# Performance work log

Hardware: AMD Instinct MI355X
Metric: run time of the kernel (lower is better)

## Reference

```python
import jax, jax.numpy as jnp
import numpy as np

N, E, D, H = 50000, 800000, 128, 4
DH = D // H  # head dim = 32


def setup_inputs() -> dict:
    key = jax.random.key(0)
    ks = jax.random.split(key, 16)
    inp = {
        "node_feats": jax.random.normal(ks[0], (N, D), jnp.float32),
        "edge_feats": jax.random.normal(ks[1], (E, D), jnp.float32),
        "src": jax.random.randint(ks[2], (E,), 0, N, jnp.int32),
        "dst": jax.random.randint(ks[3], (E,), 0, N, jnp.int32),
        # MHA projections (no bias since num_input == num_output feats)
        "Wq": jax.random.normal(ks[4], (D, D), jnp.float32) / np.sqrt(D),
        "Wk": jax.random.normal(ks[5], (D, D), jnp.float32) / np.sqrt(D),
        "Wv": jax.random.normal(ks[6], (D, D), jnp.float32) / np.sqrt(D),
        "We": jax.random.normal(ks[7], (D, D), jnp.float32) / np.sqrt(D),
        # output projection (with bias)
        "O_w": jax.random.normal(ks[8], (D, D), jnp.float32) / np.sqrt(D),
        "O_b": jnp.zeros((D,), jnp.float32),
        # batch-norm affine params
        "g1n": jnp.ones((D,), jnp.float32), "b1n": jnp.zeros((D,), jnp.float32),
        "g1e": jnp.ones((D,), jnp.float32), "b1e": jnp.zeros((D,), jnp.float32),
        "g2": jnp.ones((D,), jnp.float32), "b2": jnp.zeros((D,), jnp.float32),
        # node-feats MLP (no bias)
        "W1": jax.random.normal(ks[9], (D, 2 * D), jnp.float32) / np.sqrt(D),
        "W2": jax.random.normal(ks[10], (2 * D, D), jnp.float32) / np.sqrt(2 * D),
    }
    return inp


def _batch_norm(x, gamma, beta, eps=1e-5):
    # training-style BatchNorm1d: biased variance over the batch (node/edge) dim
    mean = jnp.mean(x, axis=0)
    var = jnp.var(x, axis=0)
    return (x - mean) * jax.lax.rsqrt(var + eps) * gamma + beta


def reference(node_feats, edge_feats, src, dst, Wq, Wk, Wv, We, O_w, O_b,
              g1n, b1n, g1e, b1e, g2, b2, W1, W2):
    h_in1 = node_feats
    nf = _batch_norm(node_feats, g1n, b1n)
    ef = _batch_norm(edge_feats, g1e, b1e)

    Q = (nf @ Wq).reshape(N, H, DH)
    K = (nf @ Wk).reshape(N, H, DH)
    V = (nf @ Wv).reshape(N, H, DH)
    proj_e = (ef @ We).reshape(E, H, DH)

    # edge-wise multiplicative attention: [E, H, DH]
    score = jnp.clip(K[src] * Q[dst] / np.sqrt(DH).astype(np.float32), -5.0, 5.0) * proj_e
    s = jnp.exp(jnp.clip(jnp.sum(score, axis=-1, keepdims=True), -5.0, 5.0))  # [E, H, 1]

    # scatter-sum aggregation to destination nodes
    wV = jax.ops.segment_sum(s * V[src], dst, num_segments=N)  # [N, H, DH]
    z = jax.ops.segment_sum(s, dst, num_segments=N)            # [N, H, 1]
    h = (wV / (z + 1e-6)).reshape(N, D)

    # dropout is identity in eval mode
    h = h @ O_w + O_b
    h = h_in1 + h  # residual 1

    h_in2 = h
    h = _batch_norm(h, g2, b2)
    h = jax.nn.silu(h @ W1) @ W2  # node_feats_MLP (dropout = identity)
    h = h_in2 + h  # residual 2
    return h
```

## Files before the change

kernel.cpp:

```cpp
#include <hip/hip_runtime.h>
#include <hip/hip_bf16.h>
#include <math.h>

#define N_NODES 50000
#define N_EDGES 800000
#define DIM 128
#define NH 4

typedef __attribute__((ext_vector_type(8))) short bf16x8;
typedef __attribute__((ext_vector_type(4))) float f32x4;
typedef unsigned int uint;
typedef unsigned short ushort;

__device__ inline short f2bf(float f) {
  __hip_bfloat16 h = __float2bfloat16(f);
  return __builtin_bit_cast(short, h);
}
__device__ inline uint pack_bf2(float lo, float hi) {
  return (uint)(ushort)f2bf(lo) | ((uint)(ushort)f2bf(hi) << 16);
}
__device__ inline float bflo(uint u) { return __builtin_bit_cast(float, u << 16); }
__device__ inline float bfhi(uint u) { return __builtin_bit_cast(float, u & 0xffff0000u); }

__global__ __launch_bounds__(256) void bn_stats_kernel(
    const float* __restrict__ x, int M, float* __restrict__ out) {
  __shared__ float s_sum[DIM];
  __shared__ float s_sq[DIM];
  int t = threadIdx.x;
  if (t < DIM) { s_sum[t] = 0.f; s_sq[t] = 0.f; }
  __syncthreads();
  int c4 = (t & 31) * 4;
  int rg = t >> 5;
  float sum0=0,sum1=0,sum2=0,sum3=0, sq0=0,sq1=0,sq2=0,sq3=0;
  for (long row = (long)blockIdx.x * 8 + rg; row < M; row += (long)gridDim.x * 8) {
    float4 v = *reinterpret_cast<const float4*>(x + row * DIM + c4);
    sum0 += v.x; sq0 += v.x * v.x;
    sum1 += v.y; sq1 += v.y * v.y;
    sum2 += v.z; sq2 += v.z * v.z;
    sum3 += v.w; sq3 += v.w * v.w;
  }
  atomicAdd(&s_sum[c4 + 0], sum0); atomicAdd(&s_sq[c4 + 0], sq0);
  atomicAdd(&s_sum[c4 + 1], sum1); atomicAdd(&s_sq[c4 + 1], sq1);
  atomicAdd(&s_sum[c4 + 2], sum2); atomicAdd(&s_sq[c4 + 2], sq2);
  atomicAdd(&s_sum[c4 + 3], sum3); atomicAdd(&s_sq[c4 + 3], sq3);
  __syncthreads();
  if (t < DIM) {
    atomicAdd(&out[t], s_sum[t]);
    atomicAdd(&out[DIM + t], s_sq[t]);
  }
}

__global__ __launch_bounds__(256) void bn_stats_hist_kernel(
    const float* __restrict__ x, const int* __restrict__ dst,
    float* __restrict__ out, int* __restrict__ deg) {
  __shared__ float s_sum[DIM];
  __shared__ float s_sq[DIM];
  int t = threadIdx.x;
  if (t < DIM) { s_sum[t] = 0.f; s_sq[t] = 0.f; }
  __syncthreads();
  for (long i = (long)blockIdx.x * 256 + t; i < N_EDGES; i += (long)gridDim.x * 256) {
    atomicAdd(&deg[dst[i]], 1);
  }
  int c4 = (t & 31) * 4;
  int rg = t >> 5;
  float sum0=0,sum1=0,sum2=0,sum3=0, sq0=0,sq1=0,sq2=0,sq3=0;
  for (long row = (long)blockIdx.x * 8 + rg; row < N_EDGES; row += (long)gridDim.x * 8) {
    float4 v = *reinterpret_cast<const float4*>(x + row * DIM + c4);
    sum0 += v.x; sq0 += v.x * v.x;
    sum1 += v.y; sq1 += v.y * v.y;
    sum2 += v.z; sq2 += v.z * v.z;
    sum3 += v.w; sq3 += v.w * v.w;
  }
  atomicAdd(&s_sum[c4 + 0], sum0); atomicAdd(&s_sq[c4 + 0], sq0);
  atomicAdd(&s_sum[c4 + 1], sum1); atomicAdd(&s_sq[c4 + 1], sq1);
  atomicAdd(&s_sum[c4 + 2], sum2); atomicAdd(&s_sq[c4 + 2], sq2);
  atomicAdd(&s_sum[c4 + 3], sum3); atomicAdd(&s_sq[c4 + 3], sq3);
  __syncthreads();
  if (t < DIM) {
    atomicAdd(&out[t], s_sum[t]);
    atomicAdd(&out[DIM + t], s_sq[t]);
  }
}

__global__ __launch_bounds__(1024) void fold6_kernel(
    const float* __restrict__ Wq, const float* __restrict__ Wk,
    const float* __restrict__ Wv, const float* __restrict__ We,
    const float* __restrict__ Ow, const float* __restrict__ W2,
    const float* __restrict__ stats_n, const float* __restrict__ stats_e,
    const float* __restrict__ g1n, const float* __restrict__ b1n,
    const float* __restrict__ g1e, const float* __restrict__ b1e, float inv_s,
    short* __restrict__ WqT, short* __restrict__ WkT,
    short* __restrict__ WvT, short* __restrict__ WeT,
    short* __restrict__ OwT, short* __restrict__ W2T,
    float* __restrict__ bq, float* __restrict__ bk,
    float* __restrict__ bv, float* __restrict__ be) {
  int b = blockIdx.x;
  int t = threadIdx.x;
  if (b == 4) {
    int d = t & 127, kg = t >> 7;
#pragma unroll
    for (int j = 0; j < 16; ++j) {
      int k = kg * 16 + j;
      OwT[d * DIM + k] = f2bf(Ow[k * DIM + d]);
    }
    return;
  }
  if (b == 5) {
    int d = t & 127, kg = t >> 7;
#pragma unroll
    for (int j = 0; j < 32; ++j) {
      int k = kg * 32 + j;
      W2T[d * 256 + k] = f2bf(W2[k * DIM + d]);
    }
    return;
  }
  __shared__ float red[8][DIM];
  __shared__ float sab[DIM], sbb[DIM];
  const float* W = (b == 0) ? Wq : (b == 1) ? Wk : (b == 2) ? Wv : We;
  const float* stats = (b == 3) ? stats_e : stats_n;
  const float* gamma = (b == 3) ? g1e : g1n;
  const float* beta  = (b == 3) ? b1e : b1n;
  float M            = (b == 3) ? (float)N_EDGES : (float)N_NODES;
  float scale = (b == 1) ? inv_s : 1.f;
  short* WT = (b == 0) ? WqT : (b == 1) ? WkT : (b == 2) ? WvT : WeT;
  float* bias = (b == 0) ? bq : (b == 1) ? bk : (b == 2) ? bv : be;
  if (t < DIM) {
    float mean = stats[t] / M;
    float var = stats[DIM + t] / M - mean * mean;
    float a = gamma[t] * rsqrtf(var + 1e-5f);
    sab[t] = a;
    sbb[t] = beta[t] - mean * a;
  }
  __syncthreads();
  int d = t & 127, kg = t >> 7;
  int ct = d >> 4, lr = d & 15;
  int L = (ct >> 1) * 32 + lr * 2 + (ct & 1);
  float bacc = 0.f;
#pragma unroll
  for (int j = 0; j < 16; ++j) {
    int k = kg * 16 + j;
    float wv = W[k * DIM + L];
    WT[d * DIM + k] = f2bf(scale * sab[k] * wv);
    bacc += sbb[k] * wv;
  }
  red[kg][d] = bacc;
  __syncthreads();
  if (kg == 0) {
    float s = 0.f;
#pragma unroll
    for (int j = 0; j < 8; ++j) s += red[j][d];
    bias[d] = scale * s;
  }
}

__global__ __launch_bounds__(256) void fold_w1_kernel(
    const float* __restrict__ W1, const float* __restrict__ stats_h,
    const float* __restrict__ g2, const float* __restrict__ b2,
    short* __restrict__ W1F, float* __restrict__ bias1) {
  __shared__ float sab[DIM], sbb[DIM];
  int t = threadIdx.x;
  if (t < DIM) {
    float mean = stats_h[t] / (float)N_NODES;
    float var = stats_h[DIM + t] / (float)N_NODES - mean * mean;
    float a = g2[t] * rsqrtf(var + 1e-5f);
    sab[t] = a;
    sbb[t] = b2[t] - mean * a;
  }
  __syncthreads();
  float bacc = 0.f;
  for (int k = 0; k < DIM; ++k) {
    float wv = W1[k * 256 + t];
    W1F[t * DIM + k] = f2bf(sab[k] * wv);
    bacc += sbb[k] * wv;
  }
  bias1[t] = bacc;
}

__device__ inline void load_a_frags(const float* __restrict__ X, long m0,
                                    int lr, int lg, bf16x8 a[4]) {
#pragma unroll
  for (int ks = 0; ks < 4; ++ks) {
    const float* p = X + (m0 + lr) * DIM + ks * 32 + lg * 8;
    float4 v0 = *reinterpret_cast<const float4*>(p);
    float4 v1 = *reinterpret_cast<const float4*>(p + 4);
    bf16x8 af;
    af[0] = f2bf(v0.x); af[1] = f2bf(v0.y); af[2] = f2bf(v0.z); af[3] = f2bf(v0.w);
    af[4] = f2bf(v1.x); af[5] = f2bf(v1.y); af[6] = f2bf(v1.z); af[7] = f2bf(v1.w);
    a[ks] = af;
  }
}

__global__ __launch_bounds__(256) void qkv_mfma_kernel(
    const float* __restrict__ nf,
    const short* __restrict__ WqT, const short* __restrict__ WkT, const short* __restrict__ WvT,
    const float* __restrict__ bq, const float* __restrict__ bk, const float* __restrict__ bv,
    ushort* __restrict__ Qb, ushort* __restrict__ Kb, ushort* __restrict__ Vb) {
  int t = threadIdx.x;
  int w = t >> 6, l = t & 63;
  int lr = l & 15, lg = l >> 4;
  long m0 = (long)blockIdx.x * 64 + w * 16;
  if (m0 >= N_NODES) return;
  bf16x8 a[4];
  load_a_frags(nf, m0, lr, lg, a);
  const short* Ws[3] = {WqT, WkT, WvT};
  const float* bs[3] = {bq, bk, bv};
  ushort* Os[3] = {Qb, Kb, Vb};
#pragma unroll 1
  for (int m = 0; m < 3; ++m) {
    const short* WT = Ws[m];
    f32x4 acc[8];
#pragma unroll
    for (int ct = 0; ct < 8; ++ct) acc[ct] = (f32x4){0.f, 0.f, 0.f, 0.f};
#pragma unroll
    for (int ct = 0; ct < 8; ++ct) {
#pragma unroll
      for (int ks = 0; ks < 4; ++ks) {
        bf16x8 b = *reinterpret_cast<const bf16x8*>(WT + (ct * 16 + lr) * DIM + ks * 32 + lg * 8);
        acc[ct] = __builtin_amdgcn_mfma_f32_16x16x32_bf16(a[ks], b, acc[ct], 0, 0, 0);
      }
    }
    const float* bb = bs[m];
    ushort* O = Os[m];
#pragma unroll
    for (int h = 0; h < 4; ++h) {
      float b0 = bb[(2 * h) * 16 + lr];
      float b1 = bb[(2 * h + 1) * 16 + lr];
#pragma unroll
      for (int r = 0; r < 4; ++r) {
        uint u = pack_bf2(acc[2 * h][r] + b0, acc[2 * h + 1][r] + b1);
        *reinterpret_cast<uint*>(O + (m0 + lg * 4 + r) * DIM + h * 32 + lr * 2) = u;
      }
    }
  }
}

#define SCAN_T 1024
#define PER_T 49
__global__ __launch_bounds__(SCAN_T) void scan_kernel(
    const int* __restrict__ deg, int* __restrict__ row_start, int* __restrict__ cursor) {
  __shared__ int ps[SCAN_T];
  int t = threadIdx.x;
  int base = t * PER_T;
  int lsum = 0;
  int local[PER_T];
#pragma unroll
  for (int j = 0; j < PER_T; ++j) {
    int idx = base + j;
    int d = (idx < N_NODES) ? deg[idx] : 0;
    local[j] = lsum;
    lsum += d;
  }
  ps[t] = lsum;
  __syncthreads();
  for (int off = 1; off < SCAN_T; off <<= 1) {
    int v = (t >= off) ? ps[t - off] : 0;
    __syncthreads();
    ps[t] += v;
    __syncthreads();
  }
  int prefix = (t == 0) ? 0 : ps[t - 1];
#pragma unroll
  for (int j = 0; j < PER_T; ++j) {
    int idx = base + j;
    if (idx < N_NODES) {
      int v = prefix + local[j];
      row_start[idx] = v;
      cursor[idx] = v;
    }
  }
  if (t == SCAN_T - 1) row_start[N_NODES] = ps[SCAN_T - 1];
}

__global__ __launch_bounds__(256) void scatter_kernel(
    const int* __restrict__ src, const int* __restrict__ dst,
    int* __restrict__ cursor, int2* __restrict__ csr) {
  int i = blockIdx.x * 256 + threadIdx.x;
  int d = dst[i];
  int pos = atomicAdd(&cursor[d], 1);
  csr[pos] = make_int2(src[i], i);
}

#define ES_GRID 2048
__global__ __launch_bounds__(256) void edge_score_kernel(
    const float* __restrict__ ef,
    const int* __restrict__ src, const int* __restrict__ dst,
    const short* __restrict__ WeT, const float* __restrict__ be,
    const ushort* __restrict__ Qb, const ushort* __restrict__ Kb,
    float* __restrict__ s_out) {
  const int NT = N_EDGES / 64;
  int t = threadIdx.x;
  int w = t >> 6, l = t & 63;
  int lr = l & 15, lg = l >> 4;
  int stride = gridDim.x;
  float ber[8];
#pragma unroll
  for (int ct = 0; ct < 8; ++ct) ber[ct] = be[ct * 16 + lr];

  int tile = blockIdx.x;
  int4 s4, d4;
  f32x4 af[8];
  {
    long m0 = (long)tile * 64 + w * 16;
    long eb = m0 + lg * 4;
    s4 = *reinterpret_cast<const int4*>(src + eb);
    d4 = *reinterpret_cast<const int4*>(dst + eb);
#pragma unroll
    for (int ks = 0; ks < 4; ++ks) {
      const float* p = ef + (m0 + lr) * DIM + ks * 32 + lg * 8;
      af[2 * ks]     = __builtin_nontemporal_load(reinterpret_cast<const f32x4*>(p));
      af[2 * ks + 1] = __builtin_nontemporal_load(reinterpret_cast<const f32x4*>(p + 4));
    }
  }

#pragma unroll 2
  for (; tile < NT; tile += stride) {
    int pt = (tile + stride < NT) ? (tile + stride) : (NT - 1);
    int sn[4] = {s4.x, s4.y, s4.z, s4.w};
    int dn[4] = {d4.x, d4.y, d4.z, d4.w};
    uint Kg[4][4], Qg[4][4];
#pragma unroll
    for (int r = 0; r < 4; ++r) {
#pragma unroll
      for (int h = 0; h < 4; ++h) {
        Kg[r][h] = *reinterpret_cast<const uint*>(Kb + (long)sn[r] * DIM + h * 32 + lr * 2);
        Qg[r][h] = *reinterpret_cast<const uint*>(Qb + (long)dn[r] * DIM + h * 32 + lr * 2);
      }
    }
    long pm0 = (long)pt * 64 + w * 16;
    long peb = pm0 + lg * 4;
    int4 ns4 = *reinterpret_cast<const int4*>(src + peb);
    int4 nd4 = *reinterpret_cast<const int4*>(dst + peb);
    bf16x8 a[4];
#pragma unroll
    for (int ks = 0; ks < 4; ++ks) {
      f32x4 v0 = af[2 * ks], v1 = af[2 * ks + 1];
      bf16x8 t8;
      t8[0] = f2bf(v0.x); t8[1] = f2bf(v0.y); t8[2] = f2bf(v0.z); t8[3] = f2bf(v0.w);
      t8[4] = f2bf(v1.x); t8[5] = f2bf(v1.y); t8[6] = f2bf(v1.z); t8[7] = f2bf(v1.w);
      a[ks] = t8;
    }
    f32x4 naf[8];
#pragma unroll
    for (int ks = 0; ks < 4; ++ks) {
      const float* p = ef + (pm0 + lr) * DIM + ks * 32 + lg * 8;
      naf[2 * ks]     = __builtin_nontemporal_load(reinterpret_cast<const f32x4*>(p));
      naf[2 * ks + 1] = __builtin_nontemporal_load(reinterpret_cast<const f32x4*>(p + 4));
    }
    f32x4 acc[8];
#pragma unroll
    for (int ct = 0; ct < 8; ++ct) acc[ct] = (f32x4){0.f, 0.f, 0.f, 0.f};
#pragma unroll
    for (int ct = 0; ct < 8; ++ct) {
#pragma unroll
      for (int ks = 0; ks < 4; ++ks) {
        bf16x8 b = *reinterpret_cast<const bf16x8*>(WeT + (ct * 16 + lr) * DIM + ks * 32 + lg * 8);
        acc[ct] = __builtin_amdgcn_mfma_f32_16x16x32_bf16(a[ks], b, acc[ct], 0, 0, 0);
      }
    }
    long eb = (long)tile * 64 + w * 16 + lg * 4;
#pragma unroll
    for (int r = 0; r < 4; ++r) {
      float hs0, hs1, hs2, hs3;
      {
        float h0, h1, h2, h3;
#pragma unroll
        for (int h = 0; h < 4; ++h) {
          float k0 = bflo(Kg[r][h]), k1 = bfhi(Kg[r][h]);
          float q0 = bflo(Qg[r][h]), q1 = bfhi(Qg[r][h]);
          float pe0 = acc[2 * h][r] + ber[2 * h];
          float pe1 = acc[2 * h + 1][r] + ber[2 * h + 1];
          float v = fminf(fmaxf(k0 * q0, -5.f), 5.f) * pe0
                  + fminf(fmaxf(k1 * q1, -5.f), 5.f) * pe1;
          if (h == 0) h0 = v; else if (h == 1) h1 = v; else if (h == 2) h2 = v; else h3 = v;
        }
        hs0 = h0; hs1 = h1; hs2 = h2; hs3 = h3;
      }
#pragma unroll
      for (int m2 = 8; m2 >= 1; m2 >>= 1) {
        hs0 += __shfl_xor(hs0, m2);
        hs1 += __shfl_xor(hs1, m2);
        hs2 += __shfl_xor(hs2, m2);
        hs3 += __shfl_xor(hs3, m2);
      }
      if (lr < 4) {
        float myh = (lr == 0) ? hs0 : ((lr == 1) ? hs1 : ((lr == 2) ? hs2 : hs3));
        s_out[(eb + r) * 4 + lr] = __expf(fminf(fmaxf(myh, -5.f), 5.f));
      }
    }
    s4 = ns4; d4 = nd4;
#pragma unroll
    for (int i = 0; i < 8; ++i) af[i] = naf[i];
  }
}

__global__ __launch_bounds__(256) void aggregate_kernel(
    const int* __restrict__ row_start, const int2* __restrict__ csr,
    const float* __restrict__ s_arr, const ushort* __restrict__ Vb,
    ushort* __restrict__ haggb) {
  int t = threadIdx.x;
  int w = t >> 6, l = t & 63;
  int n = blockIdx.x * 4 + w;
  int r0 = row_start[n], r1 = row_start[n + 1];
  int h = l >> 4;
  float a0 = 0.f, a1 = 0.f, zacc = 0.f;
  int idx = r0;
  for (; idx + 4 <= r1; idx += 4) {
    int2 rec[4];
#pragma unroll
    for (int j = 0; j < 4; ++j) rec[j] = csr[idx + j];
    float sv[4]; uint uv[4];
#pragma unroll
    for (int j = 0; j < 4; ++j) {
      sv[j] = s_arr[(long)rec[j].y * 4 + h];
      uv[j] = *reinterpret_cast<const uint*>(Vb + (long)rec[j].x * DIM + l * 2);
    }
#pragma unroll
    for (int j = 0; j < 4; ++j) {
      a0 += sv[j] * bflo(uv[j]);
      a1 += sv[j] * bfhi(uv[j]);
      zacc += sv[j];
    }
  }
  for (; idx < r1; ++idx) {
    int2 ra = csr[idx];
    float sa = s_arr[(long)ra.y * 4 + h];
    uint ua = *reinterpret_cast<const uint*>(Vb + (long)ra.x * DIM + l * 2);
    a0 += sa * bflo(ua);
    a1 += sa * bfhi(ua);
    zacc += sa;
  }
  float inv = 1.f / (zacc + 1e-6f);
  *reinterpret_cast<uint*>(haggb + (long)n * DIM + l * 2) = pack_bf2(a0 * inv, a1 * inv);
}

__global__ __launch_bounds__(256) void attnout_mfma_kernel(
    const ushort* __restrict__ haggb, const short* __restrict__ OwT,
    const float* __restrict__ Ob, const float* __restrict__ h_in1,
    float* __restrict__ hres, float* __restrict__ stats2) {
  int t = threadIdx.x;
  int w = t >> 6, l = t & 63;
  int lr = l & 15, lg = l >> 4;
  long m0 = (long)blockIdx.x * 64 + w * 16;
  if (m0 >= N_NODES) return;
  bf16x8 a[4];
#pragma unroll
  for (int ks = 0; ks < 4; ++ks) {
    a[ks] = *reinterpret_cast<const bf16x8*>(haggb + (m0 + lr) * DIM + ks * 32 + lg * 8);
  }
  f32x4 acc[8];
#pragma unroll
  for (int ct = 0; ct < 8; ++ct) acc[ct] = (f32x4){0.f, 0.f, 0.f, 0.f};
#pragma unroll
  for (int ct = 0; ct < 8; ++ct) {
#pragma unroll
    for (int ks = 0; ks < 4; ++ks) {
      bf16x8 b = *reinterpret_cast<const bf16x8*>(OwT + (ct * 16 + lr) * DIM + ks * 32 + lg * 8);
      acc[ct] = __builtin_amdgcn_mfma_f32_16x16x32_bf16(a[ks], b, acc[ct], 0, 0, 0);
    }
  }
#pragma unroll
  for (int ct = 0; ct < 8; ++ct) {
    float ob = Ob[ct * 16 + lr];
    float ls = 0.f, lq = 0.f;
#pragma unroll
    for (int r = 0; r < 4; ++r) {
      long idx = (m0 + lg * 4 + r) * DIM + ct * 16 + lr;
      float hv = h_in1[idx] + acc[ct][r] + ob;
      hres[idx] = hv;
      ls += hv; lq += hv * hv;
    }
    ls += __shfl_xor(ls, 16); ls += __shfl_xor(ls, 32);
    lq += __shfl_xor(lq, 16); lq += __shfl_xor(lq, 32);
    if (lg == 0) {
      atomicAdd(&stats2[ct * 16 + lr], ls);
      atomicAdd(&stats2[DIM + ct * 16 + lr], lq);
    }
  }
}

__global__ __launch_bounds__(256) void mlp_mfma_kernel(
    const float* __restrict__ hres, const short* __restrict__ W1F,
    const float* __restrict__ bias1, const short* __restrict__ W2T,
    float* __restrict__ out) {
  __shared__ short mid[64][264];
  int t = threadIdx.x;
  int w = t >> 6, l = t & 63;
  int lr = l & 15, lg = l >> 4;
  long m0 = (long)blockIdx.x * 64 + w * 16;
  if (m0 >= N_NODES) return;
  bf16x8 a1[4];
  load_a_frags(hres, m0, lr, lg, a1);
#pragma unroll
  for (int ct = 0; ct < 16; ++ct) {
    f32x4 acc = (f32x4){0.f, 0.f, 0.f, 0.f};
#pragma unroll
    for (int ks = 0; ks < 4; ++ks) {
      bf16x8 b = *reinterpret_cast<const bf16x8*>(W1F + (ct * 16 + lr) * DIM + ks * 32 + lg * 8);
      acc = __builtin_amdgcn_mfma_f32_16x16x32_bf16(a1[ks], b, acc, 0, 0, 0);
    }
    float bb = bias1[ct * 16 + lr];
#pragma unroll
    for (int r = 0; r < 4; ++r) {
      float x = acc[r] + bb;
      float sl = x / (1.f + __expf(-x));
      mid[w * 16 + lg * 4 + r][ct * 16 + lr] = f2bf(sl);
    }
  }
  bf16x8 a2[8];
#pragma unroll
  for (int ks = 0; ks < 8; ++ks) {
    a2[ks] = *reinterpret_cast<const bf16x8*>(&mid[w * 16 + lr][ks * 32 + lg * 8]);
  }
#pragma unroll
  for (int ct = 0; ct < 8; ++ct) {
    f32x4 acc = (f32x4){0.f, 0.f, 0.f, 0.f};
#pragma unroll
    for (int ks = 0; ks < 8; ++ks) {
      bf16x8 b = *reinterpret_cast<const bf16x8*>(W2T + (ct * 16 + lr) * 256 + ks * 32 + lg * 8);
      acc = __builtin_amdgcn_mfma_f32_16x16x32_bf16(a2[ks], b, acc, 0, 0, 0);
    }
#pragma unroll
    for (int r = 0; r < 4; ++r) {
      long idx = (m0 + lg * 4 + r) * DIM + ct * 16 + lr;
      out[idx] = hres[idx] + acc[r];
    }
  }
}

extern "C" void kernel_launch(void* const* d_in, const int* in_sizes, int n_in,
                              void* d_out, int out_size, void* d_ws, size_t ws_size,
                              hipStream_t stream) {
  const float* node_feats = (const float*)d_in[0];
  const float* edge_feats = (const float*)d_in[1];
  const int* src = (const int*)d_in[2];
  const int* dst = (const int*)d_in[3];
  const float* Wq = (const float*)d_in[4];
  const float* Wk = (const float*)d_in[5];
  const float* Wv = (const float*)d_in[6];
  const float* We = (const float*)d_in[7];
  const float* Ow = (const float*)d_in[8];
  const float* Ob = (const float*)d_in[9];
  const float* g1n = (const float*)d_in[10];
  const float* b1n = (const float*)d_in[11];
  const float* g1e = (const float*)d_in[12];
  const float* b1e = (const float*)d_in[13];
  const float* g2 = (const float*)d_in[14];
  const float* b2 = (const float*)d_in[15];
  const float* W1 = (const float*)d_in[16];
  const float* W2 = (const float*)d_in[17];
  float* out = (float*)d_out;
  float* w = (float*)d_ws;

  float* stats_n = w + 0;
  float* stats_e = w + 256;
  float* stats_h = w + 512;
  float* bq = w + 1536;
  float* bk = w + 1664;
  float* bv = w + 1792;
  float* be = w + 1920;
  short* WqT = (short*)(w + 2048);
  short* WkT = (short*)(w + 10240);
  short* WvT = (short*)(w + 18432);
  short* WeT = (short*)(w + 26624);
  short* OwT = (short*)(w + 34816);
  short* W1F = (short*)(w + 43008);
  short* W2T = (short*)(w + 59392);
  float* bias1 = w + 75776;
  ushort* Qb = (ushort*)(w + 76032);
  ushort* Kb = (ushort*)(w + 3276032);
  ushort* Vb = (ushort*)(w + 6476032);
  float* s_arr = w + 9676032;
  int* deg = (int*)(w + 12876032);
  int* row_start = deg + 50048;
  int* cursor = row_start + 50064;
  int2* csr = (int2*)(cursor + 50048);
  ushort* haggb = (ushort*)(w + 76032);

  const float inv_s = 0.17677669529663687f;

  hipMemsetAsync(w, 0, 768 * sizeof(float), stream);
  hipMemsetAsync(deg, 0, 50000 * sizeof(int), stream);

  bn_stats_kernel<<<512, 256, 0, stream>>>(node_feats, N_NODES, stats_n);
  bn_stats_hist_kernel<<<2048, 256, 0, stream>>>(edge_feats, dst, stats_e, deg);
  fold6_kernel<<<6, 1024, 0, stream>>>(Wq, Wk, Wv, We, Ow, W2, stats_n, stats_e,
                                       g1n, b1n, g1e, b1e, inv_s,
                                       WqT, WkT, WvT, WeT, OwT, W2T, bq, bk, bv, be);
  scan_kernel<<<1, SCAN_T, 0, stream>>>(deg, row_start, cursor);
  scatter_kernel<<<N_EDGES / 256, 256, 0, stream>>>(src, dst, cursor, csr);

  qkv_mfma_kernel<<<(N_NODES + 63) / 64, 256, 0, stream>>>(
      node_feats, WqT, WkT, WvT, bq, bk, bv, Qb, Kb, Vb);
  edge_score_kernel<<<ES_GRID, 256, 0, stream>>>(
      edge_feats, src, dst, WeT, be, Qb, Kb, s_arr);
  aggregate_kernel<<<N_NODES / 4, 256, 0, stream>>>(row_start, csr, s_arr, Vb, haggb);
  attnout_mfma_kernel<<<(N_NODES + 63) / 64, 256, 0, stream>>>(
      haggb, OwT, Ob, node_feats, out, stats_h);
  fold_w1_kernel<<<1, 256, 0, stream>>>(W1, stats_h, g2, b2, W1F, bias1);
  mlp_mfma_kernel<<<(N_NODES + 63) / 64, 256, 0, stream>>>(out, W1F, bias1, W2T, out);
}
```

Measured before the change: 814.4 us.

## Deepen edge-score gather pipeline and parallelize W1 folding across blocks

The edge score loop now software-pipelines the Q/K gathers one tile ahead and the src/dst index loads two tiles ahead, so random gather latency overlaps the current tile's MFMA work. The edge-feature prefetch writes directly into the live register buffer instead of a temporary copy. The W1 fold kernel is spread from one block to 16 blocks, each reducing partial bias sums in shared memory, to shorten a serial single-block step. The deeper pipeline raises register pressure and may reduce occupancy.

```diff
diff --git a/kernel.cpp b/kernel.cpp
--- a/kernel.cpp
+++ b/kernel.cpp
@@ -158,6 +158,7 @@
     const float* __restrict__ g2, const float* __restrict__ b2,
     short* __restrict__ W1F, float* __restrict__ bias1) {
   __shared__ float sab[DIM], sbb[DIM];
+  __shared__ float red[16][17];
   int t = threadIdx.x;
   if (t < DIM) {
     float mean = stats_h[t] / (float)N_NODES;
@@ -167,13 +168,24 @@
     sbb[t] = b2[t] - mean * a;
   }
   __syncthreads();
+  int dl = t & 15, kg = t >> 4;
+  int d = blockIdx.x * 16 + dl;
   float bacc = 0.f;
-  for (int k = 0; k < DIM; ++k) {
-    float wv = W1[k * 256 + t];
-    W1F[t * DIM + k] = f2bf(sab[k] * wv);
+#pragma unroll
+  for (int j = 0; j < 8; ++j) {
+    int k = kg * 8 + j;
+    float wv = W1[k * 256 + d];
+    W1F[d * DIM + k] = f2bf(sab[k] * wv);
     bacc += sbb[k] * wv;
   }
-  bias1[t] = bacc;
+  red[dl][kg] = bacc;
+  __syncthreads();
+  if (kg == 0) {
+    float s = 0.f;
+#pragma unroll
+    for (int j = 0; j < 16; ++j) s += red[dl][j];
+    bias1[d] = s;
+  }
 }
 
 __device__ inline void load_a_frags(const float* __restrict__ X, long m0,
@@ -297,13 +309,12 @@
   for (int ct = 0; ct < 8; ++ct) ber[ct] = be[ct * 16 + lr];
 
   int tile = blockIdx.x;
-  int4 s4, d4;
+  long sb0 = (long)tile * 64 + w * 16 + lg * 4;
+  int4 s4 = *reinterpret_cast<const int4*>(src + sb0);
+  int4 d4 = *reinterpret_cast<const int4*>(dst + sb0);
   f32x4 af[8];
   {
     long m0 = (long)tile * 64 + w * 16;
-    long eb = m0 + lg * 4;
-    s4 = *reinterpret_cast<const int4*>(src + eb);
-    d4 = *reinterpret_cast<const int4*>(dst + eb);
 #pragma unroll
     for (int ks = 0; ks < 4; ++ks) {
       const float* p = ef + (m0 + lr) * DIM + ks * 32 + lg * 8;
@@ -311,25 +322,28 @@
       af[2 * ks + 1] = __builtin_nontemporal_load(reinterpret_cast<const f32x4*>(p + 4));
     }
   }
-
-#pragma unroll 2
-  for (; tile < NT; tile += stride) {
-    int pt = (tile + stride < NT) ? (tile + stride) : (NT - 1);
+  uint KgA[4][4], QgA[4][4];
+  {
     int sn[4] = {s4.x, s4.y, s4.z, s4.w};
     int dn[4] = {d4.x, d4.y, d4.z, d4.w};
-    uint Kg[4][4], Qg[4][4];
 #pragma unroll
     for (int r = 0; r < 4; ++r) {
 #pragma unroll
       for (int h = 0; h < 4; ++h) {
-        Kg[r][h] = *reinterpret_cast<const uint*>(Kb + (long)sn[r] * DIM + h * 32 + lr * 2);
-        Qg[r][h] = *reinterpret_cast<const uint*>(Qb + (long)dn[r] * DIM + h * 32 + lr * 2);
-      }
-    }
-    long pm0 = (long)pt * 64 + w * 16;
-    long peb = pm0 + lg * 4;
-    int4 ns4 = *reinterpret_cast<const int4*>(src + peb);
-    int4 nd4 = *reinterpret_cast<const int4*>(dst + peb);
+        KgA[r][h] = *reinterpret_cast<const uint*>(Kb + (long)sn[r] * DIM + h * 32 + lr * 2);
+        QgA[r][h] = *reinterpret_cast<const uint*>(Qb + (long)dn[r] * DIM + h * 32 + lr * 2);
+      }
+    }
+  }
+  int t1 = (tile + stride < NT) ? tile + stride : NT - 1;
+  long sb1 = (long)t1 * 64 + w * 16 + lg * 4;
+  int4 s4n = *reinterpret_cast<const int4*>(src + sb1);
+  int4 d4n = *reinterpret_cast<const int4*>(dst + sb1);
+
+  for (; tile < NT; tile += stride) {
+    int ptile = (tile + stride < NT) ? tile + stride : NT - 1;
+    int pptile = (tile + 2 * stride < NT) ? tile + 2 * stride : NT - 1;
+    long pm0 = (long)ptile * 64 + w * 16;
     bf16x8 a[4];
 #pragma unroll
     for (int ks = 0; ks < 4; ++ks) {
@@ -339,13 +353,28 @@
       t8[4] = f2bf(v1.x); t8[5] = f2bf(v1.y); t8[6] = f2bf(v1.z); t8[7] = f2bf(v1.w);
       a[ks] = t8;
     }
-    f32x4 naf[8];
 #pragma unroll
     for (int ks = 0; ks < 4; ++ks) {
       const float* p = ef + (pm0 + lr) * DIM + ks * 32 + lg * 8;
-      naf[2 * ks]     = __builtin_nontemporal_load(reinterpret_cast<const f32x4*>(p));
-      naf[2 * ks + 1] = __builtin_nontemporal_load(reinterpret_cast<const f32x4*>(p + 4));
-    }
+      af[2 * ks]     = __builtin_nontemporal_load(reinterpret_cast<const f32x4*>(p));
+      af[2 * ks + 1] = __builtin_nontemporal_load(reinterpret_cast<const f32x4*>(p + 4));
+    }
+    uint KgB[4][4], QgB[4][4];
+    {
+      int sn[4] = {s4n.x, s4n.y, s4n.z, s4n.w};
+      int dn[4] = {d4n.x, d4n.y, d4n.z, d4n.w};
+#pragma unroll
+      for (int r = 0; r < 4; ++r) {
+#pragma unroll
+        for (int h = 0; h < 4; ++h) {
+          KgB[r][h] = *reinterpret_cast<const uint*>(Kb + (long)sn[r] * DIM + h * 32 + lr * 2);
+          QgB[r][h] = *reinterpret_cast<const uint*>(Qb + (long)dn[r] * DIM + h * 32 + lr * 2);
+        }
+      }
+    }
+    long sb2 = (long)pptile * 64 + w * 16 + lg * 4;
+    int4 s4nn = *reinterpret_cast<const int4*>(src + sb2);
+    int4 d4nn = *reinterpret_cast<const int4*>(dst + sb2);
     f32x4 acc[8];
 #pragma unroll
     for (int ct = 0; ct < 8; ++ct) acc[ct] = (f32x4){0.f, 0.f, 0.f, 0.f};
@@ -365,8 +394,8 @@
         float h0, h1, h2, h3;
 #pragma unroll
         for (int h = 0; h < 4; ++h) {
-          float k0 = bflo(Kg[r][h]), k1 = bfhi(Kg[r][h]);
-          float q0 = bflo(Qg[r][h]), q1 = bfhi(Qg[r][h]);
+          float k0 = bflo(KgA[r][h]), k1 = bfhi(KgA[r][h]);
+          float q0 = bflo(QgA[r][h]), q1 = bfhi(QgA[r][h]);
           float pe0 = acc[2 * h][r] + ber[2 * h];
           float pe1 = acc[2 * h + 1][r] + ber[2 * h + 1];
           float v = fminf(fmaxf(k0 * q0, -5.f), 5.f) * pe0
@@ -387,9 +416,12 @@
         s_out[(eb + r) * 4 + lr] = __expf(fminf(fmaxf(myh, -5.f), 5.f));
       }
     }
-    s4 = ns4; d4 = nd4;
-#pragma unroll
-    for (int i = 0; i < 8; ++i) af[i] = naf[i];
+#pragma unroll
+    for (int r = 0; r < 4; ++r) {
+#pragma unroll
+      for (int h = 0; h < 4; ++h) { KgA[r][h] = KgB[r][h]; QgA[r][h] = QgB[r][h]; }
+    }
+    s4n = s4nn; d4n = d4nn;
   }
 }
 
@@ -596,6 +628,6 @@
   aggregate_kernel<<<N_NODES / 4, 256, 0, stream>>>(row_start, csr, s_arr, Vb, haggb);
   attnout_mfma_kernel<<<(N_NODES + 63) / 64, 256, 0, stream>>>(
       haggb, OwT, Ob, node_feats, out, stats_h);
-  fold_w1_kernel<<<1, 256, 0, stream>>>(W1, stats_h, g2, b2, W1F, bias1);
+  fold_w1_kernel<<<16, 256, 0, stream>>>(W1, stats_h, g2, b2, W1F, bias1);
   mlp_mfma_kernel<<<(N_NODES + 63) / 64, 256, 0, stream>>>(out, W1F, bias1, W2T, out);
 }
```

Result: no change. 815.1 us (+0.1%).

## Process edges in CSR order and parallelize W1 folding across blocks

Applied to the files above, without the earlier changes.

The scatter kernel now writes an int4 record (src, edge id, dst) per CSR slot. The edge-score kernel walks edges in dst-sorted CSR order, chunked per XCD, so consecutive edges share Q rows and it writes scores contiguously in CSR order. The aggregate kernel can then read scores sequentially instead of gathering them by edge id. In exchange, edge features are now gathered by edge id instead of streamed, the ef prefetch pipelining is removed, and the CSR array doubles in size. The W1 fold is also split across 16 blocks with a shared-memory reduction of the bias.

```diff
diff --git a/kernel.cpp b/kernel.cpp
--- a/kernel.cpp
+++ b/kernel.cpp
@@ -158,6 +158,7 @@
     const float* __restrict__ g2, const float* __restrict__ b2,
     short* __restrict__ W1F, float* __restrict__ bias1) {
   __shared__ float sab[DIM], sbb[DIM];
+  __shared__ float red[16][17];
   int t = threadIdx.x;
   if (t < DIM) {
     float mean = stats_h[t] / (float)N_NODES;
@@ -167,13 +168,24 @@
     sbb[t] = b2[t] - mean * a;
   }
   __syncthreads();
+  int dl = t & 15, kg = t >> 4;
+  int d = blockIdx.x * 16 + dl;
   float bacc = 0.f;
-  for (int k = 0; k < DIM; ++k) {
-    float wv = W1[k * 256 + t];
-    W1F[t * DIM + k] = f2bf(sab[k] * wv);
+#pragma unroll
+  for (int j = 0; j < 8; ++j) {
+    int k = kg * 8 + j;
+    float wv = W1[k * 256 + d];
+    W1F[d * DIM + k] = f2bf(sab[k] * wv);
     bacc += sbb[k] * wv;
   }
-  bias1[t] = bacc;
+  red[dl][kg] = bacc;
+  __syncthreads();
+  if (kg == 0) {
+    float s = 0.f;
+#pragma unroll
+    for (int j = 0; j < 16; ++j) s += red[dl][j];
+    bias1[d] = s;
+  }
 }
 
 __device__ inline void load_a_frags(const float* __restrict__ X, long m0,
@@ -273,50 +285,42 @@
 
 __global__ __launch_bounds__(256) void scatter_kernel(
     const int* __restrict__ src, const int* __restrict__ dst,
-    int* __restrict__ cursor, int2* __restrict__ csr) {
+    int* __restrict__ cursor, int4* __restrict__ csr4) {
   int i = blockIdx.x * 256 + threadIdx.x;
   int d = dst[i];
   int pos = atomicAdd(&cursor[d], 1);
-  csr[pos] = make_int2(src[i], i);
+  csr4[pos] = make_int4(src[i], i, d, 0);
 }
 
 #define ES_GRID 2048
 __global__ __launch_bounds__(256) void edge_score_kernel(
     const float* __restrict__ ef,
-    const int* __restrict__ src, const int* __restrict__ dst,
+    const int4* __restrict__ csr4,
     const short* __restrict__ WeT, const float* __restrict__ be,
     const ushort* __restrict__ Qb, const ushort* __restrict__ Kb,
-    float* __restrict__ s_out) {
+    float* __restrict__ s_csr) {
   const int NT = N_EDGES / 64;
+  const int CHUNK = (NT + 7) / 8;
   int t = threadIdx.x;
   int w = t >> 6, l = t & 63;
   int lr = l & 15, lg = l >> 4;
-  int stride = gridDim.x;
+  int bid = blockIdx.x;
+  int xcd = bid & 7, j0 = bid >> 3;
+  int start = xcd * CHUNK + j0;
+  int end = ((xcd + 1) * CHUNK < NT) ? (xcd + 1) * CHUNK : NT;
   float ber[8];
 #pragma unroll
   for (int ct = 0; ct < 8; ++ct) ber[ct] = be[ct * 16 + lr];
 
-  int tile = blockIdx.x;
-  int4 s4, d4;
-  f32x4 af[8];
-  {
-    long m0 = (long)tile * 64 + w * 16;
-    long eb = m0 + lg * 4;
-    s4 = *reinterpret_cast<const int4*>(src + eb);
-    d4 = *reinterpret_cast<const int4*>(dst + eb);
-#pragma unroll
-    for (int ks = 0; ks < 4; ++ks) {
-      const float* p = ef + (m0 + lr) * DIM + ks * 32 + lg * 8;
-      af[2 * ks]     = __builtin_nontemporal_load(reinterpret_cast<const f32x4*>(p));
-      af[2 * ks + 1] = __builtin_nontemporal_load(reinterpret_cast<const f32x4*>(p + 4));
-    }
-  }
-
-#pragma unroll 2
-  for (; tile < NT; tile += stride) {
-    int pt = (tile + stride < NT) ? (tile + stride) : (NT - 1);
-    int sn[4] = {s4.x, s4.y, s4.z, s4.w};
-    int dn[4] = {d4.x, d4.y, d4.z, d4.w};
+  for (int tile = start; tile < end; tile += 256) {
+    long base = (long)tile * 64 + w * 16;
+    int4 ent = csr4[base + lr];
+    int sn[4], dn[4];
+#pragma unroll
+    for (int r = 0; r < 4; ++r) {
+      sn[r] = __shfl(ent.x, lg * 4 + r);
+      dn[r] = __shfl(ent.z, lg * 4 + r);
+    }
     uint Kg[4][4], Qg[4][4];
 #pragma unroll
     for (int r = 0; r < 4; ++r) {
@@ -326,25 +330,19 @@
         Qg[r][h] = *reinterpret_cast<const uint*>(Qb + (long)dn[r] * DIM + h * 32 + lr * 2);
       }
     }
-    long pm0 = (long)pt * 64 + w * 16;
-    long peb = pm0 + lg * 4;
-    int4 ns4 = *reinterpret_cast<const int4*>(src + peb);
-    int4 nd4 = *reinterpret_cast<const int4*>(dst + peb);
     bf16x8 a[4];
-#pragma unroll
-    for (int ks = 0; ks < 4; ++ks) {
-      f32x4 v0 = af[2 * ks], v1 = af[2 * ks + 1];
-      bf16x8 t8;
-      t8[0] = f2bf(v0.x); t8[1] = f2bf(v0.y); t8[2] = f2bf(v0.z); t8[3] = f2bf(v0.w);
-      t8[4] = f2bf(v1.x); t8[5] = f2bf(v1.y); t8[6] = f2bf(v1.z); t8[7] = f2bf(v1.w);
-      a[ks] = t8;
-    }
-    f32x4 naf[8];
-#pragma unroll
-    for (int ks = 0; ks < 4; ++ks) {
-      const float* p = ef + (pm0 + lr) * DIM + ks * 32 + lg * 8;
-      naf[2 * ks]     = __builtin_nontemporal_load(reinterpret_cast<const f32x4*>(p));
-      naf[2 * ks + 1] = __builtin_nontemporal_load(reinterpret_cast<const f32x4*>(p + 4));
+    {
+      const float* rowp = ef + (long)ent.y * DIM;
+#pragma unroll
+      for (int ks = 0; ks < 4; ++ks) {
+        const float* p = rowp + ks * 32 + lg * 8;
+        f32x4 v0 = *reinterpret_cast<const f32x4*>(p);
+        f32x4 v1 = *reinterpret_cast<const f32x4*>(p + 4);
+        bf16x8 t8;
+        t8[0] = f2bf(v0.x); t8[1] = f2bf(v0.y); t8[2] = f2bf(v0.z); t8[3] = f2bf(v0.w);
+        t8[4] = f2bf(v1.x); t8[5] = f2bf(v1.y); t8[6] = f2bf(v1.z); t8[7] = f2bf(v1.w);
+        a[ks] = t8;
+      }
     }
     f32x4 acc[8];
 #pragma unroll
@@ -357,7 +355,6 @@
         acc[ct] = __builtin_amdgcn_mfma_f32_16x16x32_bf16(a[ks], b, acc[ct], 0, 0, 0);
       }
     }
-    long eb = (long)tile * 64 + w * 16 + lg * 4;
 #pragma unroll
     for (int r = 0; r < 4; ++r) {
       float hs0, hs1, hs2, hs3;
@@ -384,18 +381,15 @@
       }
       if (lr < 4) {
         float myh = (lr == 0) ? hs0 : ((lr == 1) ? hs1 : ((lr == 2) ? hs2 : hs3));
-        s_out[(eb + r) * 4 + lr] = __expf(fminf(fmaxf(myh, -5.f), 5.f));
-      }
-    }
-    s4 = ns4; d4 = nd4;
-#pragma unroll
-    for (int i = 0; i < 8; ++i) af[i] = naf[i];
+        s_csr[(base + lg * 4 + r) * 4 + lr] = __expf(fminf(fmaxf(myh, -5.f), 5.f));
+      }
+    }
   }
 }
 
 __global__ __launch_bounds__(256) void aggregate_kernel(
-    const int* __restrict__ row_start, const int2* __restrict__ csr,
-    const float* __restrict__ s_arr, const ushort* __restrict__ Vb,
+    const int* __restrict__ row_start, const int4* __restrict__ csr4,
+    const float* __restrict__ s_csr, const ushort* __restrict__ Vb,
     ushort* __restrict__ haggb) {
   int t = threadIdx.x;
   int w = t >> 6, l = t & 63;
@@ -405,26 +399,25 @@
   float a0 = 0.f, a1 = 0.f, zacc = 0.f;
   int idx = r0;
   for (; idx + 4 <= r1; idx += 4) {
-    int2 rec[4];
-#pragma unroll
-    for (int j = 0; j < 4; ++j) rec[j] = csr[idx + j];
-    float sv[4]; uint uv[4];
-#pragma unroll
-    for (int j = 0; j < 4; ++j) {
-      sv[j] = s_arr[(long)rec[j].y * 4 + h];
-      uv[j] = *reinterpret_cast<const uint*>(Vb + (long)rec[j].x * DIM + l * 2);
-    }
-#pragma unroll
-    for (int j = 0; j < 4; ++j) {
-      a0 += sv[j] * bflo(uv[j]);
-      a1 += sv[j] * bfhi(uv[j]);
-      zacc += sv[j];
+    int sn[4]; float sv[4]; uint uv[4];
+#pragma unroll
+    for (int jj = 0; jj < 4; ++jj) sn[jj] = csr4[idx + jj].x;
+#pragma unroll
+    for (int jj = 0; jj < 4; ++jj) {
+      sv[jj] = s_csr[(long)(idx + jj) * 4 + h];
+      uv[jj] = *reinterpret_cast<const uint*>(Vb + (long)sn[jj] * DIM + l * 2);
+    }
+#pragma unroll
+    for (int jj = 0; jj < 4; ++jj) {
+      a0 += sv[jj] * bflo(uv[jj]);
+      a1 += sv[jj] * bfhi(uv[jj]);
+      zacc += sv[jj];
     }
   }
   for (; idx < r1; ++idx) {
-    int2 ra = csr[idx];
-    float sa = s_arr[(long)ra.y * 4 + h];
-    uint ua = *reinterpret_cast<const uint*>(Vb + (long)ra.x * DIM + l * 2);
+    int sn = csr4[idx].x;
+    float sa = s_csr[(long)idx * 4 + h];
+    uint ua = *reinterpret_cast<const uint*>(Vb + (long)sn * DIM + l * 2);
     a0 += sa * bflo(ua);
     a1 += sa * bfhi(ua);
     zacc += sa;
@@ -569,11 +562,11 @@
   ushort* Qb = (ushort*)(w + 76032);
   ushort* Kb = (ushort*)(w + 3276032);
   ushort* Vb = (ushort*)(w + 6476032);
-  float* s_arr = w + 9676032;
+  float* s_csr = w + 9676032;
   int* deg = (int*)(w + 12876032);
   int* row_start = deg + 50048;
   int* cursor = row_start + 50064;
-  int2* csr = (int2*)(cursor + 50048);
+  int4* csr4 = (int4*)(w + 13026192);
   ushort* haggb = (ushort*)(w + 76032);
 
   const float inv_s = 0.17677669529663687f;
@@ -587,15 +580,15 @@
                                        g1n, b1n, g1e, b1e, inv_s,
                                        WqT, WkT, WvT, WeT, OwT, W2T, bq, bk, bv, be);
   scan_kernel<<<1, SCAN_T, 0, stream>>>(deg, row_start, cursor);
-  scatter_kernel<<<N_EDGES / 256, 256, 0, stream>>>(src, dst, cursor, csr);
+  scatter_kernel<<<N_EDGES / 256, 256, 0, stream>>>(src, dst, cursor, csr4);
 
   qkv_mfma_kernel<<<(N_NODES + 63) / 64, 256, 0, stream>>>(
       node_feats, WqT, WkT, WvT, bq, bk, bv, Qb, Kb, Vb);
   edge_score_kernel<<<ES_GRID, 256, 0, stream>>>(
-      edge_feats, src, dst, WeT, be, Qb, Kb, s_arr);
-  aggregate_kernel<<<N_NODES / 4, 256, 0, stream>>>(row_start, csr, s_arr, Vb, haggb);
+      edge_feats, csr4, WeT, be, Qb, Kb, s_csr);
+  aggregate_kernel<<<N_NODES / 4, 256, 0, stream>>>(row_start, csr4, s_csr, Vb, haggb);
   attnout_mfma_kernel<<<(N_NODES + 63) / 64, 256, 0, stream>>>(
       haggb, OwT, Ob, node_feats, out, stats_h);
-  fold_w1_kernel<<<1, 256, 0, stream>>>(W1, stats_h, g2, b2, W1F, bias1);
+  fold_w1_kernel<<<16, 256, 0, stream>>>(W1, stats_h, g2, b2, W1F, bias1);
   mlp_mfma_kernel<<<(N_NODES + 63) / 64, 256, 0, stream>>>(out, W1F, bias1, W2T, out);
 }
```

New measurement: 841.5 us. 1.03x slower.

## Convert edge feats to bf16 during stats pass, merge stats kernels, parallelize W1 fold

Applied to the files above, without the earlier changes.

The edge-feature statistics pass now also writes a bf16 copy of edge_feats. The edge score kernel reads that half-size copy instead of re-reading fp32 edge_feats, which lets its software prefetch pipeline be removed. The two stats kernels are merged into a single launch, and the W1 fold is spread over 16 blocks with a shared-memory reduction instead of running in one block. This trades an extra ~200MB write plus a 200MB bf16 read against a 400MB fp32 re-read, and adds workspace usage.

```diff
diff --git a/kernel.cpp b/kernel.cpp
--- a/kernel.cpp
+++ b/kernel.cpp
@@ -22,8 +22,11 @@
 __device__ inline float bflo(uint u) { return __builtin_bit_cast(float, u << 16); }
 __device__ inline float bfhi(uint u) { return __builtin_bit_cast(float, u & 0xffff0000u); }
 
-__global__ __launch_bounds__(256) void bn_stats_kernel(
-    const float* __restrict__ x, int M, float* __restrict__ out) {
+__global__ __launch_bounds__(256) void stats_all_kernel(
+    const float* __restrict__ nf, const float* __restrict__ ef,
+    const int* __restrict__ dst,
+    float* __restrict__ stats_n, float* __restrict__ stats_e,
+    int* __restrict__ deg, ushort* __restrict__ efb) {
   __shared__ float s_sum[DIM];
   __shared__ float s_sq[DIM];
   int t = threadIdx.x;
@@ -32,53 +35,48 @@
   int c4 = (t & 31) * 4;
   int rg = t >> 5;
   float sum0=0,sum1=0,sum2=0,sum3=0, sq0=0,sq1=0,sq2=0,sq3=0;
-  for (long row = (long)blockIdx.x * 8 + rg; row < M; row += (long)gridDim.x * 8) {
-    float4 v = *reinterpret_cast<const float4*>(x + row * DIM + c4);
-    sum0 += v.x; sq0 += v.x * v.x;
-    sum1 += v.y; sq1 += v.y * v.y;
-    sum2 += v.z; sq2 += v.z * v.z;
-    sum3 += v.w; sq3 += v.w * v.w;
-  }
-  atomicAdd(&s_sum[c4 + 0], sum0); atomicAdd(&s_sq[c4 + 0], sq0);
-  atomicAdd(&s_sum[c4 + 1], sum1); atomicAdd(&s_sq[c4 + 1], sq1);
-  atomicAdd(&s_sum[c4 + 2], sum2); atomicAdd(&s_sq[c4 + 2], sq2);
-  atomicAdd(&s_sum[c4 + 3], sum3); atomicAdd(&s_sq[c4 + 3], sq3);
-  __syncthreads();
-  if (t < DIM) {
-    atomicAdd(&out[t], s_sum[t]);
-    atomicAdd(&out[DIM + t], s_sq[t]);
-  }
-}
-
-__global__ __launch_bounds__(256) void bn_stats_hist_kernel(
-    const float* __restrict__ x, const int* __restrict__ dst,
-    float* __restrict__ out, int* __restrict__ deg) {
-  __shared__ float s_sum[DIM];
-  __shared__ float s_sq[DIM];
-  int t = threadIdx.x;
-  if (t < DIM) { s_sum[t] = 0.f; s_sq[t] = 0.f; }
-  __syncthreads();
-  for (long i = (long)blockIdx.x * 256 + t; i < N_EDGES; i += (long)gridDim.x * 256) {
-    atomicAdd(&deg[dst[i]], 1);
-  }
-  int c4 = (t & 31) * 4;
-  int rg = t >> 5;
-  float sum0=0,sum1=0,sum2=0,sum3=0, sq0=0,sq1=0,sq2=0,sq3=0;
-  for (long row = (long)blockIdx.x * 8 + rg; row < N_EDGES; row += (long)gridDim.x * 8) {
-    float4 v = *reinterpret_cast<const float4*>(x + row * DIM + c4);
-    sum0 += v.x; sq0 += v.x * v.x;
-    sum1 += v.y; sq1 += v.y * v.y;
-    sum2 += v.z; sq2 += v.z * v.z;
-    sum3 += v.w; sq3 += v.w * v.w;
-  }
-  atomicAdd(&s_sum[c4 + 0], sum0); atomicAdd(&s_sq[c4 + 0], sq0);
-  atomicAdd(&s_sum[c4 + 1], sum1); atomicAdd(&s_sq[c4 + 1], sq1);
-  atomicAdd(&s_sum[c4 + 2], sum2); atomicAdd(&s_sq[c4 + 2], sq2);
-  atomicAdd(&s_sum[c4 + 3], sum3); atomicAdd(&s_sq[c4 + 3], sq3);
-  __syncthreads();
-  if (t < DIM) {
-    atomicAdd(&out[t], s_sum[t]);
-    atomicAdd(&out[DIM + t], s_sq[t]);
+  if (blockIdx.x < 512) {
+    for (long row = (long)blockIdx.x * 8 + rg; row < N_NODES; row += 512L * 8) {
+      float4 v = *reinterpret_cast<const float4*>(nf + row * DIM + c4);
+      sum0 += v.x; sq0 += v.x * v.x;
+      sum1 += v.y; sq1 += v.y * v.y;
+      sum2 += v.z; sq2 += v.z * v.z;
+      sum3 += v.w; sq3 += v.w * v.w;
+    }
+    atomicAdd(&s_sum[c4 + 0], sum0); atomicAdd(&s_sq[c4 + 0], sq0);
+    atomicAdd(&s_sum[c4 + 1], sum1); atomicAdd(&s_sq[c4 + 1], sq1);
+    atomicAdd(&s_sum[c4 + 2], sum2); atomicAdd(&s_sq[c4 + 2], sq2);
+    atomicAdd(&s_sum[c4 + 3], sum3); atomicAdd(&s_sq[c4 + 3], sq3);
+    __syncthreads();
+    if (t < DIM) {
+      atomicAdd(&stats_n[t], s_sum[t]);
+      atomicAdd(&stats_n[DIM + t], s_sq[t]);
+    }
+  } else {
+    long bid2 = blockIdx.x - 512;
+    for (long i = bid2 * 256 + t; i < N_EDGES; i += 2048L * 256) {
+      atomicAdd(&deg[dst[i]], 1);
+    }
+    for (long row = bid2 * 8 + rg; row < N_EDGES; row += 2048L * 8) {
+      float4 v = *reinterpret_cast<const float4*>(ef + row * DIM + c4);
+      sum0 += v.x; sq0 += v.x * v.x;
+      sum1 += v.y; sq1 += v.y * v.y;
+      sum2 += v.z; sq2 += v.z * v.z;
+      sum3 += v.w; sq3 += v.w * v.w;
+      uint2 p;
+      p.x = pack_bf2(v.x, v.y);
+      p.y = pack_bf2(v.z, v.w);
+      *reinterpret_cast<uint2*>(efb + row * DIM + c4) = p;
+    }
+    atomicAdd(&s_sum[c4 + 0], sum0); atomicAdd(&s_sq[c4 + 0], sq0);
+    atomicAdd(&s_sum[c4 + 1], sum1); atomicAdd(&s_sq[c4 + 1], sq1);
+    atomicAdd(&s_sum[c4 + 2], sum2); atomicAdd(&s_sq[c4 + 2], sq2);
+    atomicAdd(&s_sum[c4 + 3], sum3); atomicAdd(&s_sq[c4 + 3], sq3);
+    __syncthreads();
+    if (t < DIM) {
+      atomicAdd(&stats_e[t], s_sum[t]);
+      atomicAdd(&stats_e[DIM + t], s_sq[t]);
+    }
   }
 }
 
@@ -158,6 +156,7 @@
     const float* __restrict__ g2, const float* __restrict__ b2,
     short* __restrict__ W1F, float* __restrict__ bias1) {
   __shared__ float sab[DIM], sbb[DIM];
+  __shared__ float red[16][17];
   int t = threadIdx.x;
   if (t < DIM) {
     float mean = stats_h[t] / (float)N_NODES;
@@ -167,13 +166,24 @@
     sbb[t] = b2[t] - mean * a;
   }
   __syncthreads();
+  int dl = t & 15, kg = t >> 4;
+  int d = blockIdx.x * 16 + dl;
   float bacc = 0.f;
-  for (int k = 0; k < DIM; ++k) {
-    float wv = W1[k * 256 + t];
-    W1F[t * DIM + k] = f2bf(sab[k] * wv);
+#pragma unroll
+  for (int j = 0; j < 8; ++j) {
+    int k = kg * 8 + j;
+    float wv = W1[k * 256 + d];
+    W1F[d * DIM + k] = f2bf(sab[k] * wv);
     bacc += sbb[k] * wv;
   }
-  bias1[t] = bacc;
+  red[dl][kg] = bacc;
+  __syncthreads();
+  if (kg == 0) {
+    float s = 0.f;
+#pragma unroll
+    for (int j = 0; j < 16; ++j) s += red[dl][j];
+    bias1[d] = s;
+  }
 }
 
 __device__ inline void load_a_frags(const float* __restrict__ X, long m0,
@@ -282,7 +292,7 @@
 
 #define ES_GRID 2048
 __global__ __launch_bounds__(256) void edge_score_kernel(
-    const float* __restrict__ ef,
+    const ushort* __restrict__ efb,
     const int* __restrict__ src, const int* __restrict__ dst,
     const short* __restrict__ WeT, const float* __restrict__ be,
     const ushort* __restrict__ Qb, const ushort* __restrict__ Kb,
@@ -291,30 +301,15 @@
   int t = threadIdx.x;
   int w = t >> 6, l = t & 63;
   int lr = l & 15, lg = l >> 4;
-  int stride = gridDim.x;
   float ber[8];
 #pragma unroll
   for (int ct = 0; ct < 8; ++ct) ber[ct] = be[ct * 16 + lr];
 
-  int tile = blockIdx.x;
-  int4 s4, d4;
-  f32x4 af[8];
-  {
+  for (int tile = blockIdx.x; tile < NT; tile += gridDim.x) {
     long m0 = (long)tile * 64 + w * 16;
     long eb = m0 + lg * 4;
-    s4 = *reinterpret_cast<const int4*>(src + eb);
-    d4 = *reinterpret_cast<const int4*>(dst + eb);
-#pragma unroll
-    for (int ks = 0; ks < 4; ++ks) {
-      const float* p = ef + (m0 + lr) * DIM + ks * 32 + lg * 8;
-      af[2 * ks]     = __builtin_nontemporal_load(reinterpret_cast<const f32x4*>(p));
-      af[2 * ks + 1] = __builtin_nontemporal_load(reinterpret_cast<const f32x4*>(p + 4));
-    }
-  }
-
-#pragma unroll 2
-  for (; tile < NT; tile += stride) {
-    int pt = (tile + stride < NT) ? (tile + stride) : (NT - 1);
+    int4 s4 = *reinterpret_cast<const int4*>(src + eb);
+    int4 d4 = *reinterpret_cast<const int4*>(dst + eb);
     int sn[4] = {s4.x, s4.y, s4.z, s4.w};
     int dn[4] = {d4.x, d4.y, d4.z, d4.w};
     uint Kg[4][4], Qg[4][4];
@@ -326,25 +321,10 @@
         Qg[r][h] = *reinterpret_cast<const uint*>(Qb + (long)dn[r] * DIM + h * 32 + lr * 2);
       }
     }
-    long pm0 = (long)pt * 64 + w * 16;
-    long peb = pm0 + lg * 4;
-    int4 ns4 = *reinterpret_cast<const int4*>(src + peb);
-    int4 nd4 = *reinterpret_cast<const int4*>(dst + peb);
     bf16x8 a[4];
 #pragma unroll
     for (int ks = 0; ks < 4; ++ks) {
-      f32x4 v0 = af[2 * ks], v1 = af[2 * ks + 1];
-      bf16x8 t8;
-      t8[0] = f2bf(v0.x); t8[1] = f2bf(v0.y); t8[2] = f2bf(v0.z); t8[3] = f2bf(v0.w);
-      t8[4] = f2bf(v1.x); t8[5] = f2bf(v1.y); t8[6] = f2bf(v1.z); t8[7] = f2bf(v1.w);
-      a[ks] = t8;
-    }
-    f32x4 naf[8];
-#pragma unroll
-    for (int ks = 0; ks < 4; ++ks) {
-      const float* p = ef + (pm0 + lr) * DIM + ks * 32 + lg * 8;
-      naf[2 * ks]     = __builtin_nontemporal_load(reinterpret_cast<const f32x4*>(p));
-      naf[2 * ks + 1] = __builtin_nontemporal_load(reinterpret_cast<const f32x4*>(p + 4));
+      a[ks] = *reinterpret_cast<const bf16x8*>(efb + (m0 + lr) * DIM + ks * 32 + lg * 8);
     }
     f32x4 acc[8];
 #pragma unroll
@@ -357,7 +337,6 @@
         acc[ct] = __builtin_amdgcn_mfma_f32_16x16x32_bf16(a[ks], b, acc[ct], 0, 0, 0);
       }
     }
-    long eb = (long)tile * 64 + w * 16 + lg * 4;
 #pragma unroll
     for (int r = 0; r < 4; ++r) {
       float hs0, hs1, hs2, hs3;
@@ -387,9 +366,6 @@
         s_out[(eb + r) * 4 + lr] = __expf(fminf(fmaxf(myh, -5.f), 5.f));
       }
     }
-    s4 = ns4; d4 = nd4;
-#pragma unroll
-    for (int i = 0; i < 8; ++i) af[i] = naf[i];
   }
 }
 
@@ -574,6 +550,7 @@
   int* row_start = deg + 50048;
   int* cursor = row_start + 50064;
   int2* csr = (int2*)(cursor + 50048);
+  ushort* efb = (ushort*)(w + 16226192);
   ushort* haggb = (ushort*)(w + 76032);
 
   const float inv_s = 0.17677669529663687f;
@@ -581,8 +558,8 @@
   hipMemsetAsync(w, 0, 768 * sizeof(float), stream);
   hipMemsetAsync(deg, 0, 50000 * sizeof(int), stream);
 
-  bn_stats_kernel<<<512, 256, 0, stream>>>(node_feats, N_NODES, stats_n);
-  bn_stats_hist_kernel<<<2048, 256, 0, stream>>>(edge_feats, dst, stats_e, deg);
+  stats_all_kernel<<<2560, 256, 0, stream>>>(
+      node_feats, edge_feats, dst, stats_n, stats_e, deg, efb);
   fold6_kernel<<<6, 1024, 0, stream>>>(Wq, Wk, Wv, We, Ow, W2, stats_n, stats_e,
                                        g1n, b1n, g1e, b1e, inv_s,
                                        WqT, WkT, WvT, WeT, OwT, W2T, bq, bk, bv, be);
@@ -592,10 +569,10 @@
   qkv_mfma_kernel<<<(N_NODES + 63) / 64, 256, 0, stream>>>(
       node_feats, WqT, WkT, WvT, bq, bk, bv, Qb, Kb, Vb);
   edge_score_kernel<<<ES_GRID, 256, 0, stream>>>(
-      edge_feats, src, dst, WeT, be, Qb, Kb, s_arr);
+      efb, src, dst, WeT, be, Qb, Kb, s_arr);
   aggregate_kernel<<<N_NODES / 4, 256, 0, stream>>>(row_start, csr, s_arr, Vb, haggb);
   attnout_mfma_kernel<<<(N_NODES + 63) / 64, 256, 0, stream>>>(
       haggb, OwT, Ob, node_feats, out, stats_h);
-  fold_w1_kernel<<<1, 256, 0, stream>>>(W1, stats_h, g2, b2, W1F, bias1);
+  fold_w1_kernel<<<16, 256, 0, stream>>>(W1, stats_h, g2, b2, W1F, bias1);
   mlp_mfma_kernel<<<(N_NODES + 63) / 64, 256, 0, stream>>>(out, W1F, bias1, W2T, out);
 }
```

Measured after the change: 815.2 us. About the same (+0.1%).
